# Kernel tuning notes

Measured on AMD Instinct MI355X. Metric: run time of the kernel, lower is better.

The kernel has to match this reference:

```python
import jax, jax.numpy as jnp
import numpy as np

B, C, H, W = 4, 512, 64, 64
C8 = C // 8


def _proj(x, w, b):
    # fused 1x1 conv + (eval-mode) BN as per-channel affine: [o,c] x [b,c,h,w]
    return jnp.einsum('oc,bchw->bohw', w, x) + b[None, :, None, None]


def setup_inputs() -> dict:
    key = jax.random.key(0)
    ks = jax.random.split(key, 16)
    s_qk = 1.0 / np.sqrt(C)
    inp = {
        'x': jax.random.normal(ks[0], (B, C, H, W), jnp.float32),
        'pam_wq': jax.random.normal(ks[1], (C8, C), jnp.float32) * s_qk,
        'pam_bq': jax.random.normal(ks[2], (C8,), jnp.float32) * 0.02,
        'pam_wk': jax.random.normal(ks[3], (C8, C), jnp.float32) * s_qk,
        'pam_bk': jax.random.normal(ks[4], (C8,), jnp.float32) * 0.02,
        'pam_wv': jax.random.normal(ks[5], (C, C), jnp.float32) * s_qk,
        'pam_bv': jax.random.normal(ks[6], (C,), jnp.float32) * 0.02,
        'pam_gamma': jax.random.normal(ks[7], (1,), jnp.float32) * 0.1,
        'cam_wq': jax.random.normal(ks[8], (C8, C), jnp.float32) * s_qk,
        'cam_bq': jax.random.normal(ks[9], (C8,), jnp.float32) * 0.02,
        'cam_wk': jax.random.normal(ks[10], (C8, C), jnp.float32) * s_qk,
        'cam_bk': jax.random.normal(ks[11], (C8,), jnp.float32) * 0.02,
        'cam_wv': jax.random.normal(ks[12], (C, C), jnp.float32) * s_qk,
        'cam_bv': jax.random.normal(ks[13], (C,), jnp.float32) * 0.02,
        'cam_gamma': jax.random.normal(ks[14], (1,), jnp.float32) * 0.1,
    }
    return inp


def _pam(x, wq, bq, wk, bk, wv, bv, gamma):
    b, c, h, w = x.shape
    n = h * w
    q = _proj(x, wq, bq).reshape(b, -1, n)              # [B,C8,N]
    k = _proj(x, wk, bk).reshape(b, -1, n)              # [B,C8,N]
    energy = jnp.einsum('bdq,bdk->bqk', q, k)           # [B,N,N]
    attn = jax.nn.softmax(energy, axis=-1)
    v = _proj(x, wv, bv).reshape(b, c, n)               # [B,C,N]
    out = jnp.einsum('bck,bqk->bcq', v, attn).reshape(b, c, h, w)
    return gamma * out + x


def _cam(x, wq, bq, wk, bk, wv, bv, gamma):
    b, c, h, w = x.shape
    n = h * w
    # note: conv outputs [B,C/8,H,W] but original views it as (B, C, -1)
    q = _proj(x, wq, bq).reshape(b, c, -1)              # [B,C,N/8]
    k = _proj(x, wk, bk).reshape(b, c, -1)              # [B,C,N/8]
    energy = jnp.einsum('bcm,bdm->bcd', q, k)           # [B,C,C]
    energy_new = jnp.max(energy, axis=-1, keepdims=True) - energy
    attn = jax.nn.softmax(energy_new, axis=-1)
    v = _proj(x, wv, bv).reshape(b, c, n)               # [B,C,N]
    out = jnp.einsum('bcd,bdn->bcn', attn, v).reshape(b, c, h, w)
    return gamma * out + x


def reference(x, pam_wq, pam_bq, pam_wk, pam_bk, pam_wv, pam_bv, pam_gamma,
              cam_wq, cam_bq, cam_wk, cam_bk, cam_wv, cam_bv, cam_gamma):
    sa = _pam(x, pam_wq, pam_bq, pam_wk, pam_bk, pam_wv, pam_bv, pam_gamma)
    sc = _cam(x, cam_wq, cam_bq, cam_wk, cam_bk, cam_wv, cam_bv, cam_gamma)
    return sa + sc
```

## Files before the change

kernel.cpp:

```cpp
#include <hip/hip_runtime.h>
#include <cstdint>

#define BB 4
#define CC 512
#define DD 64
#define NN 4096
#define KCH 512

typedef unsigned short u16;
typedef __attribute__((ext_vector_type(8))) short bf16x8;
typedef __attribute__((ext_vector_type(4))) float f32x4;
typedef __attribute__((ext_vector_type(8))) unsigned short us8;

__device__ __forceinline__ float bf2f(u16 u) {
  union { unsigned int i; float f; } v; v.i = ((unsigned int)u) << 16; return v.f;
}
__device__ __forceinline__ u16 f2bf(float f) {
  unsigned int x = __float_as_uint(f);
  if ((x & 0x7fffffffu) > 0x7f800000u) return (u16)0x7fc0;
  return (u16)((x + 0x7fffu + ((x >> 16) & 1u)) >> 16);
}

__global__ __launch_bounds__(256) void zero_kernel(float* __restrict__ p, int n) {
  int i = blockIdx.x * 256 + threadIdx.x;
  if (i < n) p[i] = 0.f;
}

__global__ __launch_bounds__(256) void proj_kernel(
    const float* __restrict__ W, const float* __restrict__ bias,
    const float* __restrict__ X, u16* __restrict__ out, int O)
{
  const int b = blockIdx.z;
  const int o0 = blockIdx.y << 6;
  const int n0 = blockIdx.x << 6;
  const int t = threadIdx.x;
  const int tx = t & 15, ty = t >> 4;
  __shared__ float Wt[32][65];
  __shared__ float Xt[32][64];
  float acc[4][4];
#pragma unroll
  for (int i = 0; i < 4; ++i) {
    float bv = bias[o0 + ty * 4 + i];
    acc[i][0] = bv; acc[i][1] = bv; acc[i][2] = bv; acc[i][3] = bv;
  }
  const float* Xb = X + (size_t)b * CC * NN;
  for (int c0 = 0; c0 < CC; c0 += 32) {
#pragma unroll
    for (int i = 0; i < 8; ++i) {
      int lin = t + (i << 8);
      int c = lin & 31, o = lin >> 5;
      Wt[c][o] = W[(o0 + o) * CC + c0 + c];
    }
#pragma unroll
    for (int i = 0; i < 8; ++i) {
      int lin = t + (i << 8);
      int c = lin >> 6, n = lin & 63;
      Xt[c][n] = Xb[(c0 + c) * NN + n0 + n];
    }
    __syncthreads();
#pragma unroll
    for (int c = 0; c < 32; ++c) {
      float4 xv = *(const float4*)&Xt[c][tx * 4];
#pragma unroll
      for (int i = 0; i < 4; ++i) {
        float wv = Wt[c][ty * 4 + i];
        acc[i][0] += wv * xv.x; acc[i][1] += wv * xv.y;
        acc[i][2] += wv * xv.z; acc[i][3] += wv * xv.w;
      }
    }
    __syncthreads();
  }
  u16* ob = out + ((size_t)b * O + o0) * NN;
#pragma unroll
  for (int i = 0; i < 4; ++i) {
    ushort4 s;
    s.x = f2bf(acc[i][0]); s.y = f2bf(acc[i][1]);
    s.z = f2bf(acc[i][2]); s.w = f2bf(acc[i][3]);
    *(ushort4*)&ob[(ty * 4 + i) * NN + n0 + tx * 4] = s;
  }
}

__global__ __launch_bounds__(256) void projT_mfma_kernel(
    const float* __restrict__ W, const float* __restrict__ bias,
    const float* __restrict__ X, u16* __restrict__ oT)
{
  const int b = blockIdx.z;
  const int n0 = blockIdx.x * 128;
  const int t = threadIdx.x;
  const int lane = t & 63, wid = t >> 6;
  const int g = lane >> 4, l15 = lane & 15;
  __shared__ __align__(16) u16 XT[128][72];
  __shared__ __align__(16) u16 WT[64][72];
  const float* Xb = X + (size_t)b * CC * NN;
  f32x4 acc[2][4] = {};
  for (int c0 = 0; c0 < CC; c0 += 64) {
#pragma unroll
    for (int i = 0; i < 4; ++i) {
      int idx = t + 256 * i;
      int o = idx >> 4, cq = (idx & 15) * 4;
      float4 w = *(const float4*)&W[(size_t)o * CC + c0 + cq];
      ushort4 s; s.x = f2bf(w.x); s.y = f2bf(w.y); s.z = f2bf(w.z); s.w = f2bf(w.w);
      *(ushort4*)&WT[o][cq] = s;
    }
#pragma unroll
    for (int i = 0; i < 4; ++i) {
      int idx = t + 256 * i;
      int n4 = (idx & 31) * 4, cp = idx >> 5;
      float4 v0 = *(const float4*)&Xb[(size_t)(c0 + 2 * cp) * NN + n0 + n4];
      float4 v1 = *(const float4*)&Xb[(size_t)(c0 + 2 * cp + 1) * NN + n0 + n4];
      float a0[4] = {v0.x, v0.y, v0.z, v0.w};
      float a1[4] = {v1.x, v1.y, v1.z, v1.w};
#pragma unroll
      for (int j = 0; j < 4; ++j) {
        int jr = (j + (idx & 31)) & 3;
        uint32_t pk = (uint32_t)f2bf(a0[jr]) | ((uint32_t)f2bf(a1[jr]) << 16);
        *(uint32_t*)&XT[n4 + jr][2 * cp] = pk;
      }
    }
    __syncthreads();
#pragma unroll
    for (int ks = 0; ks < 2; ++ks) {
      bf16x8 bfr[4];
#pragma unroll
      for (int nt = 0; nt < 4; ++nt)
        bfr[nt] = *(const bf16x8*)&WT[16 * nt + l15][32 * ks + 8 * g];
#pragma unroll
      for (int mt = 0; mt < 2; ++mt) {
        bf16x8 a = *(const bf16x8*)&XT[32 * wid + 16 * mt + l15][32 * ks + 8 * g];
#pragma unroll
        for (int nt = 0; nt < 4; ++nt)
          acc[mt][nt] = __builtin_amdgcn_mfma_f32_16x16x32_bf16(a, bfr[nt], acc[mt][nt], 0, 0, 0);
      }
    }
    __syncthreads();
  }
  u16* ob = oT + (size_t)b * NN * DD;
#pragma unroll
  for (int mt = 0; mt < 2; ++mt)
#pragma unroll
    for (int nt = 0; nt < 4; ++nt) {
      float bv = bias[16 * nt + l15];
#pragma unroll
      for (int r = 0; r < 4; ++r) {
        int n = n0 + 32 * wid + 16 * mt + 4 * g + r;
        ob[(size_t)n * DD + 16 * nt + l15] = f2bf(acc[mt][nt][r] + bv);
      }
    }
}

__global__ __launch_bounds__(256) void projV_mfma_kernel(
    const float* __restrict__ W, const float* __restrict__ bias,
    const float* __restrict__ X, u16* __restrict__ out)
{
  const int b = blockIdx.z;
  const int o0 = blockIdx.y * 128;
  const int n0 = blockIdx.x * 128;
  const int t = threadIdx.x;
  const int lane = t & 63, wid = t >> 6;
  const int g = lane >> 4, l15 = lane & 15;
  const int wm = (wid >> 1) * 64, wn = (wid & 1) * 64;
  __shared__ __align__(16) u16 WT[128][72];
  __shared__ __align__(16) u16 XT[128][72];
  const float* Xb = X + (size_t)b * CC * NN;
  f32x4 acc[4][4] = {};
  for (int c0 = 0; c0 < CC; c0 += 64) {
#pragma unroll
    for (int i = 0; i < 8; ++i) {
      int idx = t + 256 * i;
      int o = idx >> 4, cq = (idx & 15) * 4;
      float4 w = *(const float4*)&W[(size_t)(o0 + o) * CC + c0 + cq];
      ushort4 s; s.x = f2bf(w.x); s.y = f2bf(w.y); s.z = f2bf(w.z); s.w = f2bf(w.w);
      *(ushort4*)&WT[o][cq] = s;
    }
#pragma unroll
    for (int i = 0; i < 4; ++i) {
      int idx = t + 256 * i;
      int n4 = (idx & 31) * 4, cp = idx >> 5;
      float4 v0 = *(const float4*)&Xb[(size_t)(c0 + 2 * cp) * NN + n0 + n4];
      float4 v1 = *(const float4*)&Xb[(size_t)(c0 + 2 * cp + 1) * NN + n0 + n4];
      float a0[4] = {v0.x, v0.y, v0.z, v0.w};
      float a1[4] = {v1.x, v1.y, v1.z, v1.w};
#pragma unroll
      for (int j = 0; j < 4; ++j) {
        int jr = (j + (idx & 31)) & 3;
        uint32_t pk = (uint32_t)f2bf(a0[jr]) | ((uint32_t)f2bf(a1[jr]) << 16);
        *(uint32_t*)&XT[n4 + jr][2 * cp] = pk;
      }
    }
    __syncthreads();
#pragma unroll
    for (int ks = 0; ks < 2; ++ks) {
      bf16x8 af[4], bfr[4];
#pragma unroll
      for (int mt = 0; mt < 4; ++mt)
        af[mt] = *(const bf16x8*)&WT[wm + 16 * mt + l15][32 * ks + 8 * g];
#pragma unroll
      for (int nt = 0; nt < 4; ++nt)
        bfr[nt] = *(const bf16x8*)&XT[wn + 16 * nt + l15][32 * ks + 8 * g];
#pragma unroll
      for (int mt = 0; mt < 4; ++mt)
#pragma unroll
        for (int nt = 0; nt < 4; ++nt)
          acc[mt][nt] = __builtin_amdgcn_mfma_f32_16x16x32_bf16(af[mt], bfr[nt], acc[mt][nt], 0, 0, 0);
    }
    __syncthreads();
  }
#pragma unroll
  for (int mt = 0; mt < 4; ++mt)
#pragma unroll
    for (int r = 0; r < 4; ++r) {
      int o = o0 + wm + 16 * mt + 4 * g + r;
      float bv = bias[o];
      u16* orow = out + ((size_t)b * CC + o) * NN + n0 + wn;
#pragma unroll
      for (int nt = 0; nt < 4; ++nt)
        orow[16 * nt + l15] = f2bf(acc[mt][nt][r] + bv);
    }
}

__global__ __launch_bounds__(256) void pam_p_kernel(
    const u16* __restrict__ qT, const u16* __restrict__ kT,
    u16* __restrict__ P, float* __restrict__ lsum, int bbase)
{
  const int b = bbase + blockIdx.z;
  const int q0 = blockIdx.x * 32;
  const int kbase = blockIdx.y * KCH;
  const int t = threadIdx.x;
  const int lane = t & 63, wid = t >> 6;
  const int g = lane >> 4, l15 = lane & 15;
  __shared__ __align__(16) u16 QT[32][72];
  __shared__ __align__(16) u16 KT[128][72];
  __shared__ __align__(16) u16 ET[32][140];
  const u16* qTb = qT + (size_t)b * NN * DD;
  const u16* kTb = kT + (size_t)b * NN * DD;
  u16* Pb = P + (size_t)blockIdx.z * NN * NN;
  {
    int q = t >> 3, d8 = (t & 7) * 8;
    *(us8*)&QT[q][d8] = *(const us8*)&qTb[(size_t)(q0 + q) * DD + d8];
  }
  float ls[2][4] = {};
  for (int kk = 0; kk < KCH; kk += 128) {
#pragma unroll
    for (int i = 0; i < 4; ++i) {
      int idx = t + 256 * i;
      int k = idx >> 3, d8 = (idx & 7) * 8;
      *(us8*)&KT[k][d8] = *(const us8*)&kTb[(size_t)(kbase + kk + k) * DD + d8];
    }
    __syncthreads();
#pragma unroll
    for (int qt = 0; qt < 2; ++qt)
#pragma unroll
      for (int kt2 = 0; kt2 < 2; ++kt2) {
        f32x4 acc = {};
#pragma unroll
        for (int ks = 0; ks < 2; ++ks) {
          bf16x8 a = *(const bf16x8*)&QT[16 * qt + l15][32 * ks + 8 * g];
          bf16x8 bk = *(const bf16x8*)&KT[32 * wid + 16 * kt2 + l15][32 * ks + 8 * g];
          acc = __builtin_amdgcn_mfma_f32_16x16x32_bf16(a, bk, acc, 0, 0, 0);
        }
#pragma unroll
        for (int r = 0; r < 4; ++r) {
          float e = __expf(acc[r] - 20.f);
          ls[qt][r] += e;
          ET[16 * qt + 4 * g + r][32 * wid + 16 * kt2 + l15] = f2bf(e);
        }
      }
    __syncthreads();
#pragma unroll
    for (int i = 0; i < 2; ++i) {
      int idx = t + 256 * i;
      int q = idx >> 4, k8 = (idx & 15) * 8;
      *(us8*)&Pb[(size_t)(q0 + q) * NN + kbase + kk + k8] = *(const us8*)&ET[q][k8];
    }
    __syncthreads();
  }
#pragma unroll
  for (int qt = 0; qt < 2; ++qt)
#pragma unroll
    for (int r = 0; r < 4; ++r) {
      float v = ls[qt][r];
      v += __shfl_xor(v, 1); v += __shfl_xor(v, 2);
      v += __shfl_xor(v, 4); v += __shfl_xor(v, 8);
      if (l15 == 0)
        atomicAdd(&lsum[(size_t)b * NN + q0 + 16 * qt + 4 * g + r], v);
    }
}

__global__ __launch_bounds__(256) void pam_gemm_kernel(
    const u16* __restrict__ vp, const u16* __restrict__ P,
    const float* __restrict__ gamma, const float* __restrict__ X,
    const float* __restrict__ lsum, float* __restrict__ out, int bbase)
{
  const int b = bbase + blockIdx.z;
  const int c0 = blockIdx.y * 128;
  const int q0 = blockIdx.x * 128;
  const int t = threadIdx.x;
  const int lane = t & 63, wid = t >> 6;
  const int g = lane >> 4, l15 = lane & 15;
  const int wm = (wid >> 1) * 64, wn = (wid & 1) * 64;
  __shared__ __align__(16) u16 VT[128][88];
  __shared__ __align__(16) u16 PT[128][88];
  const u16* Vb = vp + (size_t)b * CC * NN;
  const u16* Pb = P + (size_t)blockIdx.z * NN * NN;
  f32x4 acc[4][4] = {};
  for (int k0 = 0; k0 < NN; k0 += 64) {
#pragma unroll
    for (int i = 0; i < 4; ++i) {
      int idx = t + 256 * i;
      int r = idx >> 3, k8 = (idx & 7) * 8;
      *(us8*)&VT[r][k8] = *(const us8*)&Vb[(size_t)(c0 + r) * NN + k0 + k8];
      *(us8*)&PT[r][k8] = *(const us8*)&Pb[(size_t)(q0 + r) * NN + k0 + k8];
    }
    __syncthreads();
#pragma unroll
    for (int ks = 0; ks < 2; ++ks) {
      bf16x8 af[4], bfr[4];
#pragma unroll
      for (int mt = 0; mt < 4; ++mt)
        af[mt] = *(const bf16x8*)&VT[wm + 16 * mt + l15][32 * ks + 8 * g];
#pragma unroll
      for (int nt = 0; nt < 4; ++nt)
        bfr[nt] = *(const bf16x8*)&PT[wn + 16 * nt + l15][32 * ks + 8 * g];
#pragma unroll
      for (int mt = 0; mt < 4; ++mt)
#pragma unroll
        for (int nt = 0; nt < 4; ++nt)
          acc[mt][nt] = __builtin_amdgcn_mfma_f32_16x16x32_bf16(
              af[mt], bfr[nt], acc[mt][nt], 0, 0, 0);
    }
    __syncthreads();
  }
  const float gv = gamma[0];
  float rl[4];
#pragma unroll
  for (int nt = 0; nt < 4; ++nt)
    rl[nt] = 1.f / lsum[(size_t)b * NN + q0 + wn + 16 * nt + l15];
#pragma unroll
  for (int mt = 0; mt < 4; ++mt) {
    int c = c0 + wm + 16 * mt + 4 * g;
#pragma unroll
    for (int r = 0; r < 4; ++r) {
      size_t rowoff = ((size_t)b * CC + c + r) * NN;
#pragma unroll
      for (int nt = 0; nt < 4; ++nt) {
        size_t off = rowoff + q0 + wn + 16 * nt + l15;
        out[off] += gv * acc[mt][nt][r] * rl[nt] + X[off];
      }
    }
  }
}

__global__ __launch_bounds__(256) void cam_energy_kernel(
    const u16* __restrict__ qc, const u16* __restrict__ kc, float* __restrict__ eC)
{
  const int b = blockIdx.z;
  const int i0 = blockIdx.y << 6;
  const int j0 = blockIdx.x << 6;
  const int t = threadIdx.x;
  const int tx = t & 15, ty = t >> 4;
  __shared__ float At[32][68];
  __shared__ float Bt[32][68];
  const u16* qb = qc + (size_t)b * CC * CC;
  const u16* kb = kc + (size_t)b * CC * CC;
  float o[4][4];
#pragma unroll
  for (int i = 0; i < 4; ++i)
#pragma unroll
    for (int j = 0; j < 4; ++j) o[i][j] = 0.f;
  for (int m0 = 0; m0 < CC; m0 += 32) {
#pragma unroll
    for (int i = 0; i < 8; ++i) {
      int lin = t + (i << 8);
      int ci = lin >> 5, m = lin & 31;
      At[m][ci] = bf2f(qb[(i0 + ci) * CC + m0 + m]);
      Bt[m][ci] = bf2f(kb[(j0 + ci) * CC + m0 + m]);
    }
    __syncthreads();
#pragma unroll
    for (int m = 0; m < 32; ++m) {
      float4 a = *(const float4*)&At[m][ty * 4];
      float4 bv = *(const float4*)&Bt[m][tx * 4];
      o[0][0] += a.x * bv.x; o[0][1] += a.x * bv.y; o[0][2] += a.x * bv.z; o[0][3] += a.x * bv.w;
      o[1][0] += a.y * bv.x; o[1][1] += a.y * bv.y; o[1][2] += a.y * bv.z; o[1][3] += a.y * bv.w;
      o[2][0] += a.z * bv.x; o[2][1] += a.z * bv.y; o[2][2] += a.z * bv.z; o[2][3] += a.z * bv.w;
      o[3][0] += a.w * bv.x; o[3][1] += a.w * bv.y; o[3][2] += a.w * bv.z; o[3][3] += a.w * bv.w;
    }
    __syncthreads();
  }
  float* eb = eC + (size_t)b * CC * CC;
#pragma unroll
  for (int i = 0; i < 4; ++i) {
    float4 v;
    v.x = o[i][0]; v.y = o[i][1]; v.z = o[i][2]; v.w = o[i][3];
    *(float4*)&eb[(i0 + ty * 4 + i) * CC + j0 + tx * 4] = v;
  }
}

__global__ __launch_bounds__(256) void cam_softmax_kernel(float* __restrict__ eC)
{
  const int b = blockIdx.y, ci = blockIdx.x;
  float* row = eC + ((size_t)b * CC + ci) * CC;
  const int t = threadIdx.x;
  float e0 = row[t], e1 = row[t + 256];
  __shared__ float red[256];
  red[t] = fminf(e0, e1);
  __syncthreads();
  for (int w = 128; w > 0; w >>= 1) {
    if (t < w) red[t] = fminf(red[t], red[t + w]);
    __syncthreads();
  }
  float rmin = red[0];
  __syncthreads();
  float p0 = __expf(rmin - e0), p1 = __expf(rmin - e1);
  red[t] = p0 + p1;
  __syncthreads();
  for (int w = 128; w > 0; w >>= 1) {
    if (t < w) red[t] += red[t + w];
    __syncthreads();
  }
  float inv = 1.f / red[0];
  row[t] = p0 * inv;
  row[t + 256] = p1 * inv;
}

__global__ __launch_bounds__(256) void cam_pv_partial_kernel(
    const float* __restrict__ attn, const u16* __restrict__ vc,
    const float* __restrict__ gamma, const float* __restrict__ X,
    float* __restrict__ outp)
{
  const int b = blockIdx.z;
  const int c00 = blockIdx.y << 6;
  const int n0 = blockIdx.x << 6;
  const int t = threadIdx.x;
  const int tx = t & 15, ty = t >> 4;
  __shared__ float At[32][68];
  __shared__ float Bt[32][64];
  const float* Ab = attn + (size_t)b * CC * CC;
  const u16* Vb = vc + (size_t)b * CC * NN;
  float o[4][4];
#pragma unroll
  for (int i = 0; i < 4; ++i)
#pragma unroll
    for (int j = 0; j < 4; ++j) o[i][j] = 0.f;
  for (int d0 = 0; d0 < CC; d0 += 32) {
#pragma unroll
    for (int i = 0; i < 8; ++i) {
      int lin = t + (i << 8);
      int c = lin >> 5, d = lin & 31;
      At[d][c] = Ab[(c00 + c) * CC + d0 + d];
    }
#pragma unroll
    for (int i = 0; i < 8; ++i) {
      int lin = t + (i << 8);
      int d = lin >> 6, n = lin & 63;
      Bt[d][n] = bf2f(Vb[(d0 + d) * NN + n0 + n]);
    }
    __syncthreads();
#pragma unroll
    for (int d = 0; d < 32; ++d) {
      float4 a = *(const float4*)&At[d][ty * 4];
      float4 bv = *(const float4*)&Bt[d][tx * 4];
      o[0][0] += a.x * bv.x; o[0][1] += a.x * bv.y; o[0][2] += a.x * bv.z; o[0][3] += a.x * bv.w;
      o[1][0] += a.y * bv.x; o[1][1] += a.y * bv.y; o[1][2] += a.y * bv.z; o[1][3] += a.y * bv.w;
      o[2][0] += a.z * bv.x; o[2][1] += a.z * bv.y; o[2][2] += a.z * bv.z; o[2][3] += a.z * bv.w;
      o[3][0] += a.w * bv.x; o[3][1] += a.w * bv.y; o[3][2] += a.w * bv.z; o[3][3] += a.w * bv.w;
    }
    __syncthreads();
  }
  float g = gamma[0];
  const float* xpb = X + ((size_t)b * CC + c00) * NN;
  float* opb = outp + ((size_t)b * CC + c00) * NN;
#pragma unroll
  for (int i = 0; i < 4; ++i) {
    size_t off = (size_t)(ty * 4 + i) * NN + n0 + tx * 4;
    float4 xv = *(const float4*)&xpb[off];
    float4 r;
    r.x = g * o[i][0] + xv.x;
    r.y = g * o[i][1] + xv.y;
    r.z = g * o[i][2] + xv.z;
    r.w = g * o[i][3] + xv.w;
    *(float4*)&opb[off] = r;
  }
}

extern "C" void kernel_launch(void* const* d_in, const int* in_sizes, int n_in,
                              void* d_out, int out_size, void* d_ws, size_t ws_size,
                              hipStream_t stream) {
  const float* x   = (const float*)d_in[0];
  const float* pwq = (const float*)d_in[1];
  const float* pbq = (const float*)d_in[2];
  const float* pwk = (const float*)d_in[3];
  const float* pbk = (const float*)d_in[4];
  const float* pwv = (const float*)d_in[5];
  const float* pbv = (const float*)d_in[6];
  const float* pgam= (const float*)d_in[7];
  const float* cwq = (const float*)d_in[8];
  const float* cbq = (const float*)d_in[9];
  const float* cwk = (const float*)d_in[10];
  const float* cbk = (const float*)d_in[11];
  const float* cwv = (const float*)d_in[12];
  const float* cbv = (const float*)d_in[13];
  const float* cgam= (const float*)d_in[14];
  float* out = (float*)d_out;

  const size_t SMALL = (size_t)BB * DD * NN;
  const size_t BIG   = (size_t)BB * CC * NN;
  u16* vbuf = (u16*)d_ws;
  u16* qbuf = vbuf + BIG;
  u16* kbuf = qbuf + SMALL;
  float* eC = (float*)(kbuf + SMALL);
  float* lsum = eC + (size_t)BB * CC * CC;
  u16* Pws = (u16*)(lsum + (size_t)BB * NN);
  size_t fixed = (size_t)((char*)Pws - (char*)d_ws);
  int NB = 1;
  if (ws_size >= fixed + 4ull * NN * NN * 2) NB = 4;
  else if (ws_size >= fixed + 2ull * NN * NN * 2) NB = 2;

  dim3 blk(256);
  proj_kernel<<<dim3(64, 1, BB), blk, 0, stream>>>(cwq, cbq, x, qbuf, DD);
  proj_kernel<<<dim3(64, 1, BB), blk, 0, stream>>>(cwk, cbk, x, kbuf, DD);
  projV_mfma_kernel<<<dim3(32, 4, BB), blk, 0, stream>>>(cwv, cbv, x, vbuf);
  cam_energy_kernel<<<dim3(8, 8, BB), blk, 0, stream>>>(qbuf, kbuf, eC);
  cam_softmax_kernel<<<dim3(CC, BB), blk, 0, stream>>>(eC);
  cam_pv_partial_kernel<<<dim3(64, 8, BB), blk, 0, stream>>>(eC, vbuf, cgam, x, out);
  projT_mfma_kernel<<<dim3(32, 1, BB), blk, 0, stream>>>(pwq, pbq, x, qbuf);
  projT_mfma_kernel<<<dim3(32, 1, BB), blk, 0, stream>>>(pwk, pbk, x, kbuf);
  projV_mfma_kernel<<<dim3(32, 4, BB), blk, 0, stream>>>(pwv, pbv, x, vbuf);
  zero_kernel<<<dim3((BB * NN) / 256), blk, 0, stream>>>(lsum, BB * NN);
  for (int bb = 0; bb < BB; bb += NB) {
    pam_p_kernel<<<dim3(NN / 32, NN / KCH, NB), blk, 0, stream>>>(qbuf, kbuf, Pws, lsum, bb);
    pam_gemm_kernel<<<dim3(NN / 128, CC / 128, NB), blk, 0, stream>>>(
        vbuf, Pws, pgam, x, lsum, out, bb);
  }
}
```

Baseline: 603.4 us.

## Move CAM branch projections, energy and attention GEMM onto bf16 MFMA

Replaces the scalar FP32 CAM kernels with bf16 MFMA kernels: the q/k projection, the channel energy GEMM and the attention-times-V GEMM. V for CAM is now written transposed (N x C) so the final GEMM can load both operands with contiguous 16-byte vector loads. The softmax writes bf16 attention into a new workspace buffer instead of overwriting the energy in place. The cost is bf16 rounding of the attention weights and the extra workspace for the bf16 attention matrix.

Measured after the change: 490.2 us. 18.8% less time.

```diff
diff --git a/kernel.cpp b/kernel.cpp
--- a/kernel.cpp
+++ b/kernel.cpp
@@ -24,60 +24,6 @@
 __global__ __launch_bounds__(256) void zero_kernel(float* __restrict__ p, int n) {
   int i = blockIdx.x * 256 + threadIdx.x;
   if (i < n) p[i] = 0.f;
-}
-
-__global__ __launch_bounds__(256) void proj_kernel(
-    const float* __restrict__ W, const float* __restrict__ bias,
-    const float* __restrict__ X, u16* __restrict__ out, int O)
-{
-  const int b = blockIdx.z;
-  const int o0 = blockIdx.y << 6;
-  const int n0 = blockIdx.x << 6;
-  const int t = threadIdx.x;
-  const int tx = t & 15, ty = t >> 4;
-  __shared__ float Wt[32][65];
-  __shared__ float Xt[32][64];
-  float acc[4][4];
-#pragma unroll
-  for (int i = 0; i < 4; ++i) {
-    float bv = bias[o0 + ty * 4 + i];
-    acc[i][0] = bv; acc[i][1] = bv; acc[i][2] = bv; acc[i][3] = bv;
-  }
-  const float* Xb = X + (size_t)b * CC * NN;
-  for (int c0 = 0; c0 < CC; c0 += 32) {
-#pragma unroll
-    for (int i = 0; i < 8; ++i) {
-      int lin = t + (i << 8);
-      int c = lin & 31, o = lin >> 5;
-      Wt[c][o] = W[(o0 + o) * CC + c0 + c];
-    }
-#pragma unroll
-    for (int i = 0; i < 8; ++i) {
-      int lin = t + (i << 8);
-      int c = lin >> 6, n = lin & 63;
-      Xt[c][n] = Xb[(c0 + c) * NN + n0 + n];
-    }
-    __syncthreads();
-#pragma unroll
-    for (int c = 0; c < 32; ++c) {
-      float4 xv = *(const float4*)&Xt[c][tx * 4];
-#pragma unroll
-      for (int i = 0; i < 4; ++i) {
-        float wv = Wt[c][ty * 4 + i];
-        acc[i][0] += wv * xv.x; acc[i][1] += wv * xv.y;
-        acc[i][2] += wv * xv.z; acc[i][3] += wv * xv.w;
-      }
-    }
-    __syncthreads();
-  }
-  u16* ob = out + ((size_t)b * O + o0) * NN;
-#pragma unroll
-  for (int i = 0; i < 4; ++i) {
-    ushort4 s;
-    s.x = f2bf(acc[i][0]); s.y = f2bf(acc[i][1]);
-    s.z = f2bf(acc[i][2]); s.w = f2bf(acc[i][3]);
-    *(ushort4*)&ob[(ty * 4 + i) * NN + n0 + tx * 4] = s;
-  }
 }
 
 __global__ __launch_bounds__(256) void projT_mfma_kernel(
@@ -216,6 +162,287 @@
       for (int nt = 0; nt < 4; ++nt)
         orow[16 * nt + l15] = f2bf(acc[mt][nt][r] + bv);
     }
+}
+
+__global__ __launch_bounds__(256) void projVT_mfma_kernel(
+    const float* __restrict__ W, const float* __restrict__ bias,
+    const float* __restrict__ X, u16* __restrict__ vT)
+{
+  const int b = blockIdx.z;
+  const int o0 = blockIdx.y * 128;
+  const int n0 = blockIdx.x * 128;
+  const int t = threadIdx.x;
+  const int lane = t & 63, wid = t >> 6;
+  const int g = lane >> 4, l15 = lane & 15;
+  const int wm = (wid >> 1) * 64, wn = (wid & 1) * 64;
+  __shared__ __align__(16) u16 WT[128][72];
+  __shared__ __align__(16) u16 XT[128][72];
+  const float* Xb = X + (size_t)b * CC * NN;
+  f32x4 acc[4][4] = {};
+  for (int c0 = 0; c0 < CC; c0 += 64) {
+#pragma unroll
+    for (int i = 0; i < 8; ++i) {
+      int idx = t + 256 * i;
+      int o = idx >> 4, cq = (idx & 15) * 4;
+      float4 w = *(const float4*)&W[(size_t)(o0 + o) * CC + c0 + cq];
+      ushort4 s; s.x = f2bf(w.x); s.y = f2bf(w.y); s.z = f2bf(w.z); s.w = f2bf(w.w);
+      *(ushort4*)&WT[o][cq] = s;
+    }
+#pragma unroll
+    for (int i = 0; i < 4; ++i) {
+      int idx = t + 256 * i;
+      int n4 = (idx & 31) * 4, cp = idx >> 5;
+      float4 v0 = *(const float4*)&Xb[(size_t)(c0 + 2 * cp) * NN + n0 + n4];
+      float4 v1 = *(const float4*)&Xb[(size_t)(c0 + 2 * cp + 1) * NN + n0 + n4];
+      float a0[4] = {v0.x, v0.y, v0.z, v0.w};
+      float a1[4] = {v1.x, v1.y, v1.z, v1.w};
+#pragma unroll
+      for (int j = 0; j < 4; ++j) {
+        int jr = (j + (idx & 31)) & 3;
+        uint32_t pk = (uint32_t)f2bf(a0[jr]) | ((uint32_t)f2bf(a1[jr]) << 16);
+        *(uint32_t*)&XT[n4 + jr][2 * cp] = pk;
+      }
+    }
+    __syncthreads();
+#pragma unroll
+    for (int ks = 0; ks < 2; ++ks) {
+      bf16x8 af[4], bfr[4];
+#pragma unroll
+      for (int mt = 0; mt < 4; ++mt)
+        af[mt] = *(const bf16x8*)&XT[wm + 16 * mt + l15][32 * ks + 8 * g];
+#pragma unroll
+      for (int nt = 0; nt < 4; ++nt)
+        bfr[nt] = *(const bf16x8*)&WT[wn + 16 * nt + l15][32 * ks + 8 * g];
+#pragma unroll
+      for (int mt = 0; mt < 4; ++mt)
+#pragma unroll
+        for (int nt = 0; nt < 4; ++nt)
+          acc[mt][nt] = __builtin_amdgcn_mfma_f32_16x16x32_bf16(af[mt], bfr[nt], acc[mt][nt], 0, 0, 0);
+    }
+    __syncthreads();
+  }
+  u16* vb = vT + (size_t)b * NN * CC;
+#pragma unroll
+  for (int mt = 0; mt < 4; ++mt)
+#pragma unroll
+    for (int r = 0; r < 4; ++r) {
+      int n = n0 + wm + 16 * mt + 4 * g + r;
+      u16* nrow = vb + (size_t)n * CC + o0 + wn;
+#pragma unroll
+      for (int nt = 0; nt < 4; ++nt)
+        nrow[16 * nt + l15] = f2bf(acc[mt][nt][r] + bias[o0 + wn + 16 * nt + l15]);
+    }
+}
+
+__global__ __launch_bounds__(256) void proj64_mfma_kernel(
+    const float* __restrict__ W, const float* __restrict__ bias,
+    const float* __restrict__ X, u16* __restrict__ out)
+{
+  const int b = blockIdx.z;
+  const int n0 = blockIdx.x * 128;
+  const int t = threadIdx.x;
+  const int lane = t & 63, wid = t >> 6;
+  const int g = lane >> 4, l15 = lane & 15;
+  const int wm = (wid >> 1) * 32, wn = (wid & 1) * 64;
+  __shared__ __align__(16) u16 WT[64][72];
+  __shared__ __align__(16) u16 XT[128][72];
+  const float* Xb = X + (size_t)b * CC * NN;
+  f32x4 acc[2][4] = {};
+  for (int c0 = 0; c0 < CC; c0 += 64) {
+#pragma unroll
+    for (int i = 0; i < 4; ++i) {
+      int idx = t + 256 * i;
+      int o = idx >> 4, cq = (idx & 15) * 4;
+      float4 w = *(const float4*)&W[(size_t)o * CC + c0 + cq];
+      ushort4 s; s.x = f2bf(w.x); s.y = f2bf(w.y); s.z = f2bf(w.z); s.w = f2bf(w.w);
+      *(ushort4*)&WT[o][cq] = s;
+    }
+#pragma unroll
+    for (int i = 0; i < 4; ++i) {
+      int idx = t + 256 * i;
+      int n4 = (idx & 31) * 4, cp = idx >> 5;
+      float4 v0 = *(const float4*)&Xb[(size_t)(c0 + 2 * cp) * NN + n0 + n4];
+      float4 v1 = *(const float4*)&Xb[(size_t)(c0 + 2 * cp + 1) * NN + n0 + n4];
+      float a0[4] = {v0.x, v0.y, v0.z, v0.w};
+      float a1[4] = {v1.x, v1.y, v1.z, v1.w};
+#pragma unroll
+      for (int j = 0; j < 4; ++j) {
+        int jr = (j + (idx & 31)) & 3;
+        uint32_t pk = (uint32_t)f2bf(a0[jr]) | ((uint32_t)f2bf(a1[jr]) << 16);
+        *(uint32_t*)&XT[n4 + jr][2 * cp] = pk;
+      }
+    }
+    __syncthreads();
+#pragma unroll
+    for (int ks = 0; ks < 2; ++ks) {
+      bf16x8 bfr[4];
+#pragma unroll
+      for (int nt = 0; nt < 4; ++nt)
+        bfr[nt] = *(const bf16x8*)&XT[wn + 16 * nt + l15][32 * ks + 8 * g];
+#pragma unroll
+      for (int mt = 0; mt < 2; ++mt) {
+        bf16x8 a = *(const bf16x8*)&WT[wm + 16 * mt + l15][32 * ks + 8 * g];
+#pragma unroll
+        for (int nt = 0; nt < 4; ++nt)
+          acc[mt][nt] = __builtin_amdgcn_mfma_f32_16x16x32_bf16(a, bfr[nt], acc[mt][nt], 0, 0, 0);
+      }
+    }
+    __syncthreads();
+  }
+  u16* ob = out + (size_t)b * DD * NN;
+#pragma unroll
+  for (int mt = 0; mt < 2; ++mt)
+#pragma unroll
+    for (int r = 0; r < 4; ++r) {
+      int o = wm + 16 * mt + 4 * g + r;
+      float bv = bias[o];
+      u16* orow = ob + (size_t)o * NN + n0 + wn;
+#pragma unroll
+      for (int nt = 0; nt < 4; ++nt)
+        orow[16 * nt + l15] = f2bf(acc[mt][nt][r] + bv);
+    }
+}
+
+__global__ __launch_bounds__(256) void cam_energy_mfma_kernel(
+    const u16* __restrict__ qc, const u16* __restrict__ kc, float* __restrict__ eC)
+{
+  const int b = blockIdx.z;
+  const int i0 = blockIdx.y * 128;
+  const int j0 = blockIdx.x * 128;
+  const int t = threadIdx.x;
+  const int lane = t & 63, wid = t >> 6;
+  const int g = lane >> 4, l15 = lane & 15;
+  const int wm = (wid >> 1) * 64, wn = (wid & 1) * 64;
+  __shared__ __align__(16) u16 QT[128][72];
+  __shared__ __align__(16) u16 KT[128][72];
+  const u16* qb = qc + (size_t)b * CC * CC;
+  const u16* kb = kc + (size_t)b * CC * CC;
+  f32x4 acc[4][4] = {};
+  for (int m0 = 0; m0 < CC; m0 += 64) {
+#pragma unroll
+    for (int i = 0; i < 4; ++i) {
+      int idx = t + 256 * i;
+      int r = idx >> 3, k8 = (idx & 7) * 8;
+      *(us8*)&QT[r][k8] = *(const us8*)&qb[(size_t)(i0 + r) * CC + m0 + k8];
+      *(us8*)&KT[r][k8] = *(const us8*)&kb[(size_t)(j0 + r) * CC + m0 + k8];
+    }
+    __syncthreads();
+#pragma unroll
+    for (int ks = 0; ks < 2; ++ks) {
+      bf16x8 af[4], bfr[4];
+#pragma unroll
+      for (int mt = 0; mt < 4; ++mt)
+        af[mt] = *(const bf16x8*)&QT[wm + 16 * mt + l15][32 * ks + 8 * g];
+#pragma unroll
+      for (int nt = 0; nt < 4; ++nt)
+        bfr[nt] = *(const bf16x8*)&KT[wn + 16 * nt + l15][32 * ks + 8 * g];
+#pragma unroll
+      for (int mt = 0; mt < 4; ++mt)
+#pragma unroll
+        for (int nt = 0; nt < 4; ++nt)
+          acc[mt][nt] = __builtin_amdgcn_mfma_f32_16x16x32_bf16(af[mt], bfr[nt], acc[mt][nt], 0, 0, 0);
+    }
+    __syncthreads();
+  }
+  float* eb = eC + (size_t)b * CC * CC;
+#pragma unroll
+  for (int mt = 0; mt < 4; ++mt)
+#pragma unroll
+    for (int r = 0; r < 4; ++r) {
+      int ci = i0 + wm + 16 * mt + 4 * g + r;
+      float* erow = eb + (size_t)ci * CC + j0 + wn;
+#pragma unroll
+      for (int nt = 0; nt < 4; ++nt)
+        erow[16 * nt + l15] = acc[mt][nt][r];
+    }
+}
+
+__global__ __launch_bounds__(256) void cam_softmax_kernel(
+    const float* __restrict__ eC, u16* __restrict__ attnB)
+{
+  const int b = blockIdx.y, ci = blockIdx.x;
+  const float* row = eC + ((size_t)b * CC + ci) * CC;
+  u16* arow = attnB + ((size_t)b * CC + ci) * CC;
+  const int t = threadIdx.x;
+  float e0 = row[t], e1 = row[t + 256];
+  __shared__ float red[256];
+  red[t] = fminf(e0, e1);
+  __syncthreads();
+  for (int w = 128; w > 0; w >>= 1) {
+    if (t < w) red[t] = fminf(red[t], red[t + w]);
+    __syncthreads();
+  }
+  float rmin = red[0];
+  __syncthreads();
+  float p0 = __expf(rmin - e0), p1 = __expf(rmin - e1);
+  red[t] = p0 + p1;
+  __syncthreads();
+  for (int w = 128; w > 0; w >>= 1) {
+    if (t < w) red[t] += red[t + w];
+    __syncthreads();
+  }
+  float inv = 1.f / red[0];
+  arow[t] = f2bf(p0 * inv);
+  arow[t + 256] = f2bf(p1 * inv);
+}
+
+__global__ __launch_bounds__(256) void cam_gemm_kernel(
+    const u16* __restrict__ attnB, const u16* __restrict__ vT,
+    const float* __restrict__ gamma, const float* __restrict__ X,
+    float* __restrict__ out)
+{
+  const int b = blockIdx.z;
+  const int c0 = blockIdx.y * 128;
+  const int n0 = blockIdx.x * 128;
+  const int t = threadIdx.x;
+  const int lane = t & 63, wid = t >> 6;
+  const int g = lane >> 4, l15 = lane & 15;
+  const int wm = (wid >> 1) * 64, wn = (wid & 1) * 64;
+  __shared__ __align__(16) u16 AT[128][72];
+  __shared__ __align__(16) u16 VTl[128][72];
+  const u16* Ab = attnB + (size_t)b * CC * CC;
+  const u16* Vb = vT + (size_t)b * NN * CC;
+  f32x4 acc[4][4] = {};
+  for (int d0 = 0; d0 < CC; d0 += 64) {
+#pragma unroll
+    for (int i = 0; i < 4; ++i) {
+      int idx = t + 256 * i;
+      int r = idx >> 3, k8 = (idx & 7) * 8;
+      *(us8*)&AT[r][k8]  = *(const us8*)&Ab[(size_t)(c0 + r) * CC + d0 + k8];
+      *(us8*)&VTl[r][k8] = *(const us8*)&Vb[(size_t)(n0 + r) * CC + d0 + k8];
+    }
+    __syncthreads();
+#pragma unroll
+    for (int ks = 0; ks < 2; ++ks) {
+      bf16x8 af[4], bfr[4];
+#pragma unroll
+      for (int mt = 0; mt < 4; ++mt)
+        af[mt] = *(const bf16x8*)&AT[wm + 16 * mt + l15][32 * ks + 8 * g];
+#pragma unroll
+      for (int nt = 0; nt < 4; ++nt)
+        bfr[nt] = *(const bf16x8*)&VTl[wn + 16 * nt + l15][32 * ks + 8 * g];
+#pragma unroll
+      for (int mt = 0; mt < 4; ++mt)
+#pragma unroll
+        for (int nt = 0; nt < 4; ++nt)
+          acc[mt][nt] = __builtin_amdgcn_mfma_f32_16x16x32_bf16(af[mt], bfr[nt], acc[mt][nt], 0, 0, 0);
+    }
+    __syncthreads();
+  }
+  const float gv = gamma[0];
+#pragma unroll
+  for (int mt = 0; mt < 4; ++mt) {
+#pragma unroll
+    for (int r = 0; r < 4; ++r) {
+      int c = c0 + wm + 16 * mt + 4 * g + r;
+      size_t rowoff = ((size_t)b * CC + c) * NN;
+#pragma unroll
+      for (int nt = 0; nt < 4; ++nt) {
+        size_t off = rowoff + n0 + wn + 16 * nt + l15;
+        out[off] = gv * acc[mt][nt][r] + X[off];
+      }
+    }
+  }
 }
 
 __global__ __launch_bounds__(256) void pam_p_kernel(
@@ -347,139 +574,6 @@
         out[off] += gv * acc[mt][nt][r] * rl[nt] + X[off];
       }
     }
-  }
-}
-
-__global__ __launch_bounds__(256) void cam_energy_kernel(
-    const u16* __restrict__ qc, const u16* __restrict__ kc, float* __restrict__ eC)
-{
-  const int b = blockIdx.z;
-  const int i0 = blockIdx.y << 6;
-  const int j0 = blockIdx.x << 6;
-  const int t = threadIdx.x;
-  const int tx = t & 15, ty = t >> 4;
-  __shared__ float At[32][68];
-  __shared__ float Bt[32][68];
-  const u16* qb = qc + (size_t)b * CC * CC;
-  const u16* kb = kc + (size_t)b * CC * CC;
-  float o[4][4];
-#pragma unroll
-  for (int i = 0; i < 4; ++i)
-#pragma unroll
-    for (int j = 0; j < 4; ++j) o[i][j] = 0.f;
-  for (int m0 = 0; m0 < CC; m0 += 32) {
-#pragma unroll
-    for (int i = 0; i < 8; ++i) {
-      int lin = t + (i << 8);
-      int ci = lin >> 5, m = lin & 31;
-      At[m][ci] = bf2f(qb[(i0 + ci) * CC + m0 + m]);
-      Bt[m][ci] = bf2f(kb[(j0 + ci) * CC + m0 + m]);
-    }
-    __syncthreads();
-#pragma unroll
-    for (int m = 0; m < 32; ++m) {
-      float4 a = *(const float4*)&At[m][ty * 4];
-      float4 bv = *(const float4*)&Bt[m][tx * 4];
-      o[0][0] += a.x * bv.x; o[0][1] += a.x * bv.y; o[0][2] += a.x * bv.z; o[0][3] += a.x * bv.w;
-      o[1][0] += a.y * bv.x; o[1][1] += a.y * bv.y; o[1][2] += a.y * bv.z; o[1][3] += a.y * bv.w;
-      o[2][0] += a.z * bv.x; o[2][1] += a.z * bv.y; o[2][2] += a.z * bv.z; o[2][3] += a.z * bv.w;
-      o[3][0] += a.w * bv.x; o[3][1] += a.w * bv.y; o[3][2] += a.w * bv.z; o[3][3] += a.w * bv.w;
-    }
-    __syncthreads();
-  }
-  float* eb = eC + (size_t)b * CC * CC;
-#pragma unroll
-  for (int i = 0; i < 4; ++i) {
-    float4 v;
-    v.x = o[i][0]; v.y = o[i][1]; v.z = o[i][2]; v.w = o[i][3];
-    *(float4*)&eb[(i0 + ty * 4 + i) * CC + j0 + tx * 4] = v;
-  }
-}
-
-__global__ __launch_bounds__(256) void cam_softmax_kernel(float* __restrict__ eC)
-{
-  const int b = blockIdx.y, ci = blockIdx.x;
-  float* row = eC + ((size_t)b * CC + ci) * CC;
-  const int t = threadIdx.x;
-  float e0 = row[t], e1 = row[t + 256];
-  __shared__ float red[256];
-  red[t] = fminf(e0, e1);
-  __syncthreads();
-  for (int w = 128; w > 0; w >>= 1) {
-    if (t < w) red[t] = fminf(red[t], red[t + w]);
-    __syncthreads();
-  }
-  float rmin = red[0];
-  __syncthreads();
-  float p0 = __expf(rmin - e0), p1 = __expf(rmin - e1);
-  red[t] = p0 + p1;
-  __syncthreads();
-  for (int w = 128; w > 0; w >>= 1) {
-    if (t < w) red[t] += red[t + w];
-    __syncthreads();
-  }
-  float inv = 1.f / red[0];
-  row[t] = p0 * inv;
-  row[t + 256] = p1 * inv;
-}
-
-__global__ __launch_bounds__(256) void cam_pv_partial_kernel(
-    const float* __restrict__ attn, const u16* __restrict__ vc,
-    const float* __restrict__ gamma, const float* __restrict__ X,
-    float* __restrict__ outp)
-{
-  const int b = blockIdx.z;
-  const int c00 = blockIdx.y << 6;
-  const int n0 = blockIdx.x << 6;
-  const int t = threadIdx.x;
-  const int tx = t & 15, ty = t >> 4;
-  __shared__ float At[32][68];
-  __shared__ float Bt[32][64];
-  const float* Ab = attn + (size_t)b * CC * CC;
-  const u16* Vb = vc + (size_t)b * CC * NN;
-  float o[4][4];
-#pragma unroll
-  for (int i = 0; i < 4; ++i)
-#pragma unroll
-    for (int j = 0; j < 4; ++j) o[i][j] = 0.f;
-  for (int d0 = 0; d0 < CC; d0 += 32) {
-#pragma unroll
-    for (int i = 0; i < 8; ++i) {
-      int lin = t + (i << 8);
-      int c = lin >> 5, d = lin & 31;
-      At[d][c] = Ab[(c00 + c) * CC + d0 + d];
-    }
-#pragma unroll
-    for (int i = 0; i < 8; ++i) {
-      int lin = t + (i << 8);
-      int d = lin >> 6, n = lin & 63;
-      Bt[d][n] = bf2f(Vb[(d0 + d) * NN + n0 + n]);
-    }
-    __syncthreads();
-#pragma unroll
-    for (int d = 0; d < 32; ++d) {
-      float4 a = *(const float4*)&At[d][ty * 4];
-      float4 bv = *(const float4*)&Bt[d][tx * 4];
-      o[0][0] += a.x * bv.x; o[0][1] += a.x * bv.y; o[0][2] += a.x * bv.z; o[0][3] += a.x * bv.w;
-      o[1][0] += a.y * bv.x; o[1][1] += a.y * bv.y; o[1][2] += a.y * bv.z; o[1][3] += a.y * bv.w;
-      o[2][0] += a.z * bv.x; o[2][1] += a.z * bv.y; o[2][2] += a.z * bv.z; o[2][3] += a.z * bv.w;
-      o[3][0] += a.w * bv.x; o[3][1] += a.w * bv.y; o[3][2] += a.w * bv.z; o[3][3] += a.w * bv.w;
-    }
-    __syncthreads();
-  }
-  float g = gamma[0];
-  const float* xpb = X + ((size_t)b * CC + c00) * NN;
-  float* opb = outp + ((size_t)b * CC + c00) * NN;
-#pragma unroll
-  for (int i = 0; i < 4; ++i) {
-    size_t off = (size_t)(ty * 4 + i) * NN + n0 + tx * 4;
-    float4 xv = *(const float4*)&xpb[off];
-    float4 r;
-    r.x = g * o[i][0] + xv.x;
-    r.y = g * o[i][1] + xv.y;
-    r.z = g * o[i][2] + xv.z;
-    r.w = g * o[i][3] + xv.w;
-    *(float4*)&opb[off] = r;
   }
 }
 
@@ -509,7 +603,8 @@
   u16* qbuf = vbuf + BIG;
   u16* kbuf = qbuf + SMALL;
   float* eC = (float*)(kbuf + SMALL);
-  float* lsum = eC + (size_t)BB * CC * CC;
+  u16* attnB = (u16*)(eC + (size_t)BB * CC * CC);
+  float* lsum = (float*)(attnB + (size_t)BB * CC * CC);
   u16* Pws = (u16*)(lsum + (size_t)BB * NN);
   size_t fixed = (size_t)((char*)Pws - (char*)d_ws);
   int NB = 1;
@@ -517,12 +612,12 @@
   else if (ws_size >= fixed + 2ull * NN * NN * 2) NB = 2;
 
   dim3 blk(256);
-  proj_kernel<<<dim3(64, 1, BB), blk, 0, stream>>>(cwq, cbq, x, qbuf, DD);
-  proj_kernel<<<dim3(64, 1, BB), blk, 0, stream>>>(cwk, cbk, x, kbuf, DD);
-  projV_mfma_kernel<<<dim3(32, 4, BB), blk, 0, stream>>>(cwv, cbv, x, vbuf);
-  cam_energy_kernel<<<dim3(8, 8, BB), blk, 0, stream>>>(qbuf, kbuf, eC);
-  cam_softmax_kernel<<<dim3(CC, BB), blk, 0, stream>>>(eC);
-  cam_pv_partial_kernel<<<dim3(64, 8, BB), blk, 0, stream>>>(eC, vbuf, cgam, x, out);
+  proj64_mfma_kernel<<<dim3(32, 1, BB), blk, 0, stream>>>(cwq, cbq, x, qbuf);
+  proj64_mfma_kernel<<<dim3(32, 1, BB), blk, 0, stream>>>(cwk, cbk, x, kbuf);
+  projVT_mfma_kernel<<<dim3(32, 4, BB), blk, 0, stream>>>(cwv, cbv, x, vbuf);
+  cam_energy_mfma_kernel<<<dim3(4, 4, BB), blk, 0, stream>>>(qbuf, kbuf, eC);
+  cam_softmax_kernel<<<dim3(CC, BB), blk, 0, stream>>>(eC, attnB);
+  cam_gemm_kernel<<<dim3(32, 4, BB), blk, 0, stream>>>(attnB, vbuf, cgam, x, out);
   projT_mfma_kernel<<<dim3(32, 1, BB), blk, 0, stream>>>(pwq, pbq, x, qbuf);
   projT_mfma_kernel<<<dim3(32, 1, BB), blk, 0, stream>>>(pwk, pbk, x, kbuf);
   projV_mfma_kernel<<<dim3(32, 4, BB), blk, 0, stream>>>(pwv, pbv, x, vbuf);
```
